# Optimization experiments

Measured on AMD Instinct MI355X. Metric: run time of the kernel, lower is better.

## Reference

```python
import jax, jax.numpy as jnp
import numpy as np

N = 6144      # total residues (12 complexes x 512)
SEG = 512
NC = 14       # atom channels per residue
E = 64        # embed_size
HD = 128      # hidden_size
C = 25        # num_classes
K = 9         # k_neighbors
L = 3         # n_layers
ROUNDS = 3    # iter_round


def _forward(X, S, batch_id, embed, W_in, b_in, channel_w, eW1, eb1, eW2, eb2, cW1, cb1, cW2, cb2, nW1, nb1, nW2, nb2, mW1, mb1, mW2, mb2, oW1, ob1, oW2, ob2):
    n = X.shape[0]
    silu = jax.nn.silu
    # pairs in different complexes (or self) are never neighbors
    cross = (batch_id[:, None] != batch_id[None, :]) | jnp.eye(n, dtype=bool)
    Hmem = None
    H = None
    for t in range(ROUNDS):
        H0 = embed[S]                                    # residue embedding [N,E]
        if Hmem is not None:                             # keep_memory: memory_ffn(H_prev)
            m = silu(Hmem) @ mW1 + mb1
            H0 = H0 + (silu(m) @ mW2 + mb2)
        H = H0 @ W_in + b_in                             # [N,HD]
        # dynamic KNN edge construction on current CA coordinates (_knn_edges)
        ca = X[:, 1]                                     # [N,3]
        d2 = jnp.sum((ca[:, None, :] - ca[None, :, :]) ** 2, -1)
        d2 = jnp.where(cross, 1e9, d2)
        _, nbr = jax.lax.top_k(-d2, K)                   # [N,K] neighbor indices
        for l in range(L):                               # AMEGNN / AMEncoder layers
            Hj = H[nbr]                                  # gather [N,K,HD]
            Xj = X[nbr]                                  # gather [N,K,NC,3]
            diff = X[:, None] - Xj                       # [N,K,NC,3]
            # channel-weighted radial feature
            radial = jnp.einsum('nkcd,nkcd,c->nk', diff, diff, channel_w)[..., None]
            Hi = jnp.broadcast_to(H[:, None], Hj.shape)
            ein = jnp.concatenate([Hi, Hj, radial], -1)  # [N,K,2HD+1]
            msg = silu(silu(ein @ eW1[l] + eb1[l]) @ eW2[l] + eb2[l])
            scale = silu(msg @ cW1[l] + cb1[l]) @ cW2[l] + cb2[l]     # [N,K,1]
            X = X + jnp.mean(diff * scale[..., None], axis=1)        # equivariant coord update
            agg = jnp.sum(msg, axis=1)                   # scatter-sum over neighbors [N,HD]
            H = H + silu(jnp.concatenate([H, agg], -1) @ nW1[l] + nb1[l]) @ nW2[l] + nb2[l]
        Hmem = H
    logits = silu(silu(H) @ oW1 + ob1) @ oW2 + ob2       # ffn_residue
    return logits, X


def setup_inputs() -> dict:
    key = jax.random.key(0)
    ks = jax.random.split(key, 16)
    r = lambda i, shape, s=0.05: jax.random.normal(ks[i], shape, dtype=jnp.float32) * s
    return {
        'X': jax.random.normal(ks[0], (N, NC, 3), dtype=jnp.float32) * 3.0,
        'S': jax.random.randint(ks[1], (N,), 0, C),
        'batch_id': jnp.arange(N, dtype=jnp.int32) // SEG,
        'embed': r(2, (C, E), 1.0),
        'W_in': r(3, (E, HD)), 'b_in': jnp.zeros((HD,), jnp.float32),
        'channel_w': jax.random.uniform(ks[4], (NC,), dtype=jnp.float32),
        'eW1': r(5, (L, 2 * HD + 1, HD)), 'eb1': jnp.zeros((L, HD), jnp.float32),
        'eW2': r(6, (L, HD, HD)), 'eb2': jnp.zeros((L, HD), jnp.float32),
        'cW1': r(7, (L, HD, HD)), 'cb1': jnp.zeros((L, HD), jnp.float32),
        'cW2': r(8, (L, HD, 1)), 'cb2': jnp.zeros((L, 1), jnp.float32),
        'nW1': r(9, (L, 2 * HD, HD)), 'nb1': jnp.zeros((L, HD), jnp.float32),
        'nW2': r(10, (L, HD, HD)), 'nb2': jnp.zeros((L, HD), jnp.float32),
        'mW1': r(11, (HD, HD)), 'mb1': jnp.zeros((HD,), jnp.float32),
        'mW2': r(12, (HD, E)), 'mb2': jnp.zeros((E,), jnp.float32),
        'oW1': r(13, (HD, HD)), 'ob1': jnp.zeros((HD,), jnp.float32),
        'oW2': r(14, (HD, C)), 'ob2': jnp.zeros((C,), jnp.float32),
    }


def reference(X, S, batch_id, embed, W_in, b_in, channel_w, eW1, eb1, eW2, eb2, cW1, cb1, cW2, cb2, nW1, nb1, nW2, nb2, mW1, mb1, mW2, mb2, oW1, ob1, oW2, ob2):
    return _forward(X, S, batch_id, embed, W_in, b_in, channel_w, eW1, eb1, eW2, eb2, cW1, cb1, cW2, cb2, nW1, nb1, nW2, nb2, mW1, mb1, mW2, mb2, oW1, ob1, oW2, ob2)
```

## Files before the change

kernel.cpp:

```cpp
#include <hip/hip_runtime.h>
#include <math.h>

#define NNODE 6144
#define SEG   512
#define NCH   14
#define XD    42
#define ED    64
#define HD    128
#define NCLS  25
#define KN    9
#define NPB   7
#define ROWS  64
#define EDGE_BLOCKS ((NNODE + NPB - 1) / NPB)

typedef __attribute__((ext_vector_type(8))) short short8;
typedef __attribute__((ext_vector_type(4))) short short4v;
typedef __attribute__((ext_vector_type(4))) float f32x4;

__device__ __forceinline__ float silu_f(float x) {
  return x / (1.0f + __expf(-x));
}
__device__ __forceinline__ short f2bf(float x) {
  unsigned u = __builtin_bit_cast(unsigned, x);
  unsigned r = (u + 0x7fffu + ((u >> 16) & 1u)) >> 16;
  return (short)r;
}
__device__ __forceinline__ float bf2f(short s) {
  unsigned u = ((unsigned)(unsigned short)s) << 16;
  return __builtin_bit_cast(float, u);
}
__device__ __forceinline__ f32x4 mfma16(short8 a, short8 b, f32x4 c) {
  return __builtin_amdgcn_mfma_f32_16x16x32_bf16(a, b, c, 0, 0, 0);
}
__device__ __forceinline__ int swz128(int row, int col) {
  return row * 128 + (col ^ ((row & 7) << 3));
}
__device__ __forceinline__ int swz256(int row, int col) {
  return row * 256 + (col ^ ((row & 7) << 3));
}
__device__ __forceinline__ int swz64(int row, int col) {
  return row * 64 + (col ^ ((row & 7) << 3));
}

#define EXOFF 344064
#define WBF_SHORTS (EXOFF + 32768)

__global__ __launch_bounds__(256) void prep_weights(
    const float* __restrict__ eW1, const float* __restrict__ eW2,
    const float* __restrict__ cW1, const float* __restrict__ nW1,
    const float* __restrict__ nW2, const float* __restrict__ mW1,
    const float* __restrict__ mW2, const float* __restrict__ W_in,
    short* __restrict__ out)
{
  const int idx = blockIdx.x * 256 + threadIdx.x;
  if (blockIdx.y == 15) {
    if (idx < 16384) {
      const int n = idx >> 7, k = idx & 127;
      out[EXOFF + idx] = f2bf(mW1[k * HD + n]);
    } else if (idx < 24576) {
      const int local = idx - 16384;
      const int n = local >> 7, k = local & 127;
      out[EXOFF + 16384 + local] = f2bf(mW2[k * ED + n]);
    } else if (idx < 32768) {
      const int local = idx - 24576;
      const int n = local >> 6, k = local & 63;
      out[EXOFF + 24576 + local] = f2bf(W_in[k * HD + n]);
    }
    return;
  }
  const int mat = blockIdx.y % 5, l = blockIdx.y / 5;
  const int K = (mat == 0 || mat == 3) ? 256 : 128;
  if (idx >= K * 128) return;
  const int n = idx / K, k = idx - n * K;
  const float* src;
  switch (mat) {
    case 0: src = eW1 + (size_t)l * 257 * 128; break;
    case 1: src = eW2 + (size_t)l * 128 * 128; break;
    case 2: src = cW1 + (size_t)l * 128 * 128; break;
    case 3: src = nW1 + (size_t)l * 256 * 128; break;
    default: src = nW2 + (size_t)l * 128 * 128; break;
  }
  const int dofs[5] = {0, 32768, 49152, 65536, 98304};
  out[(size_t)l * 114688 + dofs[mat] + idx] = f2bf(src[k * 128 + n]);
}

__global__ void copy_kernel(const float* __restrict__ src, float* __restrict__ dst, int n) {
  int i = blockIdx.x * blockDim.x + threadIdx.x;
  if (i < n) dst[i] = src[i];
}

__global__ __launch_bounds__(512) void h_init_mfma(
    const float* __restrict__ embed, const int* __restrict__ S,
    const short* __restrict__ W_inT, const float* __restrict__ b_in,
    const float* __restrict__ Hmem,
    const short* __restrict__ mW1T, const float* __restrict__ mb1,
    const short* __restrict__ mW2T, const float* __restrict__ mb2,
    const short* __restrict__ W1T0,
    float* __restrict__ Hout, short* __restrict__ PQ0)
{
  __shared__ __align__(16) short A[16 * HD];
  __shared__ __align__(16) short Bu[16 * HD];
  __shared__ __align__(16) short h0B[16 * ED];
  __shared__ __align__(16) short HB[16 * HD];
  const int t = threadIdx.x;
  const int m0 = blockIdx.x * 16;
  const int wid = t >> 6, lane = t & 63, lr = lane & 15, lk = lane >> 4;

  if (Hmem) {
    {
      const int r = t >> 5, c4 = t & 31;
      const float4 v = ((const float4*)Hmem)[(size_t)(m0 + r) * 32 + c4];
      short4v s;
      s.x = f2bf(silu_f(v.x)); s.y = f2bf(silu_f(v.y));
      s.z = f2bf(silu_f(v.z)); s.w = f2bf(silu_f(v.w));
      *(short4v*)&A[swz128(r, c4 * 4)] = s;
    }
    __syncthreads();
    {
      f32x4 acc[2] = {};
#pragma unroll
      for (int ks = 0; ks < 4; ++ks) {
        const int k0 = ks * 32 + lk * 8;
        const short8 a = *(const short8*)&A[swz128(lr, k0)];
#pragma unroll
        for (int ni = 0; ni < 2; ++ni) {
          const int c = (wid * 2 + ni) * 16 + lr;
          acc[ni] = mfma16(a, *(const short8*)(mW1T + c * 128 + k0), acc[ni]);
        }
      }
#pragma unroll
      for (int ni = 0; ni < 2; ++ni) {
        const int col = (wid * 2 + ni) * 16 + lr;
        const float bias = mb1[col];
#pragma unroll
        for (int g = 0; g < 4; ++g)
          Bu[swz128(lk * 4 + g, col)] = f2bf(silu_f(acc[ni][g] + bias));
      }
    }
    __syncthreads();
    if (wid < 4) {
      f32x4 acc = {};
#pragma unroll
      for (int ks = 0; ks < 4; ++ks) {
        const int k0 = ks * 32 + lk * 8;
        const short8 a = *(const short8*)&Bu[swz128(lr, k0)];
        const int c = wid * 16 + lr;
        acc = mfma16(a, *(const short8*)(mW2T + c * 128 + k0), acc);
      }
      const int col = wid * 16 + lr;
      const float bias = mb2[col];
#pragma unroll
      for (int g = 0; g < 4; ++g) {
        const int row = lk * 4 + g;
        h0B[swz64(row, col)] = f2bf(embed[S[m0 + row] * ED + col] + acc[g] + bias);
      }
    }
  } else {
    for (int idx = t; idx < 16 * ED; idx += 512) {
      const int row = idx >> 6, col = idx & 63;
      h0B[swz64(row, col)] = f2bf(embed[S[m0 + row] * ED + col]);
    }
  }
  __syncthreads();
  {
    f32x4 acc = {};
#pragma unroll
    for (int ks = 0; ks < 2; ++ks) {
      const int k0 = ks * 32 + lk * 8;
      const short8 a = *(const short8*)&h0B[swz64(lr, k0)];
      const int c = wid * 16 + lr;
      acc = mfma16(a, *(const short8*)(W_inT + c * 64 + k0), acc);
    }
    const int col = wid * 16 + lr;
    const float bias = b_in[col];
#pragma unroll
    for (int g = 0; g < 4; ++g) {
      const int row = lk * 4 + g;
      const float hv = acc[g] + bias;
      Hout[(size_t)(m0 + row) * HD + col] = hv;
      HB[swz128(row, col)] = f2bf(hv);
    }
  }
  __syncthreads();
  {
    f32x4 acc[2] = {};
#pragma unroll
    for (int ks = 0; ks < 4; ++ks) {
      const int k0 = ks * 32 + lk * 8;
      const short8 a = *(const short8*)&HB[swz128(lr, k0)];
#pragma unroll
      for (int ni = 0; ni < 2; ++ni) {
        const int c = (wid * 2 + ni) * 16 + lr;
        const short* bp = (c < HD) ? (W1T0 + c * 256 + k0)
                                   : (W1T0 + (c - HD) * 256 + HD + k0);
        acc[ni] = mfma16(a, *(const short8*)bp, acc[ni]);
      }
    }
#pragma unroll
    for (int ni = 0; ni < 2; ++ni) {
      const int c = (wid * 2 + ni) * 16 + lr;
#pragma unroll
      for (int g = 0; g < 4; ++g)
        PQ0[(size_t)(m0 + lk * 4 + g) * 256 + c] = f2bf(acc[ni][g]);
    }
  }
}

__global__ __launch_bounds__(512) void knn_kernel(const float* __restrict__ X,
                                                  int* __restrict__ nbr)
{
  const int w = threadIdx.x >> 6, lane = threadIdx.x & 63;
  const int i = blockIdx.x * 8 + w;
  const int base = (i / SEG) * SEG;

  const float cx = X[i * XD + 3], cy = X[i * XD + 4], cz = X[i * XD + 5];
  float dv[8];
  int   di[8];
#pragma unroll
  for (int q = 0; q < 8; ++q) {
    const int j = base + lane + q * 64;
    float dx = __fsub_rn(cx, X[j * XD + 3]);
    float dy = __fsub_rn(cy, X[j * XD + 4]);
    float dz = __fsub_rn(cz, X[j * XD + 5]);
    float d2 = __fadd_rn(__fadd_rn(__fmul_rn(dx, dx), __fmul_rn(dy, dy)), __fmul_rn(dz, dz));
    if (j == i) d2 = 1e9f;
    dv[q] = d2; di[q] = j;
  }
  for (int it = 0; it < KN; ++it) {
    float bv = dv[0]; int bi = di[0];
#pragma unroll
    for (int q = 1; q < 8; ++q)
      if (dv[q] < bv || (dv[q] == bv && di[q] < bi)) { bv = dv[q]; bi = di[q]; }
#pragma unroll
    for (int m = 1; m < 64; m <<= 1) {
      float ov = __shfl_xor(bv, m, 64);
      int   oi = __shfl_xor(bi, m, 64);
      if (ov < bv || (ov == bv && oi < bi)) { bv = ov; bi = oi; }
    }
    if (lane == 0) nbr[i * KN + it] = bi;
    const int rel = bi - base;
    const int oq = rel >> 6;
#pragma unroll
    for (int q = 0; q < 8; ++q)
      if (q == oq && (rel & 63) == lane) dv[q] = 3e38f;
  }
}

__global__ __launch_bounds__(512) void edge_layer_kernel(
    const float* __restrict__ Hin,  float* __restrict__ Hout,
    const float* __restrict__ Xin,  float* __restrict__ Xout,
    const int*   __restrict__ nbr,  const float* __restrict__ channel_w,
    const short* __restrict__ PQ,
    const float* __restrict__ eW1,  const float* __restrict__ eb1,
    const float* __restrict__ eb2,  const float* __restrict__ cb1,
    const float* __restrict__ cW2,  const float* __restrict__ cb2,
    const float* __restrict__ nb1,  const float* __restrict__ nb2,
    const short* __restrict__ W2T,  const short* __restrict__ C1T,
    const short* __restrict__ N1T,  const short* __restrict__ N2T,
    const short* __restrict__ W1Tn, short* __restrict__ PQn)
{
  __shared__ __align__(16) short bufA[ROWS * HD];
  __shared__ __align__(16) short bufB[ROWS * HD];
  __shared__ __align__(16) short nodeA[NPB * 256];
  __shared__ __align__(16) short uT[NPB * HD];
  __shared__ float diffS[ROWS][XD];
  __shared__ float scalePart[ROWS][4];
  __shared__ int   nbrS[ROWS];
  short* houtB = bufA;

  const int t  = threadIdx.x;
  const int n0 = blockIdx.x * NPB;
  const int nvalid = (NNODE - n0 < NPB) ? (NNODE - n0) : NPB;
  const int evalid = nvalid * KN;

  {
    const int row  = t >> 3;
    const int part = t & 7;
    const bool rvalid = row < evalid;
    const int nd = row / KN;
    const int jn = rvalid ? nbr[n0 * KN + row] : n0;
    if (part == 0) nbrS[row] = jn;

    float r = 0.f;
    {
      const float* xi = Xin + (size_t)(n0 + ((nd < nvalid) ? nd : 0)) * XD;
      const float* xj = Xin + (size_t)jn * XD;
#pragma unroll
      for (int ii = 0; ii < 6; ++ii) {
        const int e = part + ii * 8;
        if (e < XD) {
          float d = 0.f;
          if (rvalid) d = xi[e] - xj[e];
          diffS[row][e] = d;
          r = fmaf(channel_w[e / 3] * d, d, r);
        }
      }
    }
    r += __shfl_xor(r, 1, 64);
    r += __shfl_xor(r, 2, 64);
    r += __shfl_xor(r, 4, 64);

    if (t < NPB * (HD / 4)) {
      const int r2 = t >> 5, c4 = t & 31;
      float4 v = make_float4(0.f, 0.f, 0.f, 0.f);
      if (r2 < nvalid) v = ((const float4*)Hin)[(size_t)(n0 + r2) * 32 + c4];
      short4v s;
      s.x = f2bf(v.x); s.y = f2bf(v.y); s.z = f2bf(v.z); s.w = f2bf(v.w);
      *(short4v*)&nodeA[swz256(r2, c4 * 4)] = s;
    }

    const int inode = n0 + ((nd < nvalid) ? nd : 0);
    const short4v* PQv = (const short4v*)PQ;
    const float4* w2564 = (const float4*)(eW1 + 256 * HD);
    const float4* eb14 = (const float4*)eb1;
#pragma unroll
    for (int ii = 0; ii < 4; ++ii) {
      const int c4 = part + ii * 8;
      const short4v ps = PQv[(size_t)inode * 64 + c4];
      const short4v qs = PQv[(size_t)jn * 64 + 32 + c4];
      const float4 w = w2564[c4];
      const float4 bb = eb14[c4];
      short4v s;
      s.x = f2bf(silu_f(bf2f(ps.x) + bf2f(qs.x) + r * w.x + bb.x));
      s.y = f2bf(silu_f(bf2f(ps.y) + bf2f(qs.y) + r * w.y + bb.y));
      s.z = f2bf(silu_f(bf2f(ps.z) + bf2f(qs.z) + r * w.z + bb.z));
      s.w = f2bf(silu_f(bf2f(ps.w) + bf2f(qs.w) + r * w.w + bb.w));
      *(short4v*)&bufA[swz128(row, c4 * 4)] = s;
    }
  }
  __syncthreads();

  const int wid  = t >> 6;
  const int lane = t & 63;
  const int m2 = wid >> 2;
  const int n2 = wid & 3;
  const int lr = lane & 15;
  const int lk = lane >> 4;
  const int rA0 = (m2 * 2) * 16 + lr;
  const int rA1 = rA0 + 16;

  {
    f32x4 acc[2][2] = {};
    const short* b0p = W2T + ((n2 * 2) * 16 + lr) * 128;
    const short* b1p = b0p + 16 * 128;
#pragma unroll
    for (int ks = 0; ks < 4; ++ks) {
      const int k0 = ks * 32 + lk * 8;
      const short8 a0 = *(const short8*)&bufA[swz128(rA0, k0)];
      const short8 a1 = *(const short8*)&bufA[swz128(rA1, k0)];
      const short8 b0 = *(const short8*)(b0p + k0);
      const short8 b1 = *(const short8*)(b1p + k0);
      acc[0][0] = mfma16(a0, b0, acc[0][0]);
      acc[0][1] = mfma16(a0, b1, acc[0][1]);
      acc[1][0] = mfma16(a1, b0, acc[1][0]);
      acc[1][1] = mfma16(a1, b1, acc[1][1]);
    }
#pragma unroll
    for (int ni = 0; ni < 2; ++ni) {
      const int col = (n2 * 2 + ni) * 16 + lr;
      const float bias = eb2[col];
#pragma unroll
      for (int mi = 0; mi < 2; ++mi) {
        const int rb = (m2 * 2 + mi) * 16 + lk * 4;
#pragma unroll
        for (int g = 0; g < 4; ++g)
          bufB[swz128(rb + g, col)] = f2bf(silu_f(acc[mi][ni][g] + bias));
      }
    }
  }
  __syncthreads();

  {
    f32x4 acc[2][2] = {};
    const short* b0p = C1T + ((n2 * 2) * 16 + lr) * 128;
    const short* b1p = b0p + 16 * 128;
#pragma unroll
    for (int ks = 0; ks < 4; ++ks) {
      const int k0 = ks * 32 + lk * 8;
      const short8 a0 = *(const short8*)&bufB[swz128(rA0, k0)];
      const short8 a1 = *(const short8*)&bufB[swz128(rA1, k0)];
      const short8 b0 = *(const short8*)(b0p + k0);
      const short8 b1 = *(const short8*)(b1p + k0);
      acc[0][0] = mfma16(a0, b0, acc[0][0]);
      acc[0][1] = mfma16(a0, b1, acc[0][1]);
      acc[1][0] = mfma16(a1, b0, acc[1][0]);
      acc[1][1] = mfma16(a1, b1, acc[1][1]);
    }
    float p[2][4];
#pragma unroll
    for (int mi = 0; mi < 2; ++mi)
#pragma unroll
      for (int g = 0; g < 4; ++g) p[mi][g] = 0.f;
#pragma unroll
    for (int ni = 0; ni < 2; ++ni) {
      const int col = (n2 * 2 + ni) * 16 + lr;
      const float bias = cb1[col];
      const float wv = cW2[col];
#pragma unroll
      for (int mi = 0; mi < 2; ++mi)
#pragma unroll
        for (int g = 0; g < 4; ++g)
          p[mi][g] = fmaf(silu_f(acc[mi][ni][g] + bias), wv, p[mi][g]);
    }
#pragma unroll
    for (int m = 1; m < 16; m <<= 1) {
#pragma unroll
      for (int mi = 0; mi < 2; ++mi)
#pragma unroll
        for (int g = 0; g < 4; ++g)
          p[mi][g] += __shfl_xor(p[mi][g], m, 64);
    }
    if (lr == 0) {
#pragma unroll
      for (int mi = 0; mi < 2; ++mi)
#pragma unroll
        for (int g = 0; g < 4; ++g)
          scalePart[(m2 * 2 + mi) * 16 + lk * 4 + g][n2] = p[mi][g];
    }
  }
  for (int idx = t; idx < NPB * HD; idx += 512) {
    const int r2 = idx >> 7, col = idx & 127;
    float v = 0.f;
    if (r2 < nvalid) {
#pragma unroll
      for (int k = 0; k < KN; ++k) v += bf2f(bufB[swz128(r2 * KN + k, col)]);
    }
    nodeA[swz256(r2, col + HD)] = f2bf(v);
  }
  __syncthreads();

  {
    f32x4 acc = {};
    const short* bp = N1T + (wid * 16 + lr) * 256;
#pragma unroll
    for (int ks = 0; ks < 8; ++ks) {
      const int k0 = ks * 32 + lk * 8;
      short8 a = {0, 0, 0, 0, 0, 0, 0, 0};
      if (lr < NPB) a = *(const short8*)&nodeA[swz256(lr, k0)];
      const short8 b = *(const short8*)(bp + k0);
      acc = mfma16(a, b, acc);
    }
    const int col = wid * 16 + lr;
    const float bias = nb1[col];
#pragma unroll
    for (int g = 0; g < 4; ++g) {
      const int orow = lk * 4 + g;
      if (orow < NPB) uT[swz128(orow, col)] = f2bf(silu_f(acc[g] + bias));
    }
  }
  if (t < NPB * XD) {
    const int nd = t / XD, e = t - nd * XD;
    if (nd < nvalid) {
      const float c2 = cb2[0];
      float a = 0.f;
#pragma unroll
      for (int k = 0; k < KN; ++k) {
        const int r = nd * KN + k;
        const float sc = ((scalePart[r][0] + scalePart[r][1])
                        + (scalePart[r][2] + scalePart[r][3])) + c2;
        a = fmaf(diffS[r][e], sc, a);
      }
      const float xi = Xin[(size_t)n0 * XD + t];
      Xout[(size_t)n0 * XD + t] = xi + a / 9.0f;
    }
  }
  __syncthreads();

  {
    f32x4 acc = {};
    const short* bp = N2T + (wid * 16 + lr) * 128;
#pragma unroll
    for (int ks = 0; ks < 4; ++ks) {
      const int k0 = ks * 32 + lk * 8;
      short8 a = {0, 0, 0, 0, 0, 0, 0, 0};
      if (lr < NPB) a = *(const short8*)&uT[swz128(lr, k0)];
      const short8 b = *(const short8*)(bp + k0);
      acc = mfma16(a, b, acc);
    }
    const int col = wid * 16 + lr;
    const float bias = nb2[col];
#pragma unroll
    for (int g = 0; g < 4; ++g) {
      const int row = lk * 4 + g;
      if (row < nvalid) {
        const float hv = Hin[(size_t)(n0 + row) * HD + col] + acc[g] + bias;
        Hout[(size_t)(n0 + row) * HD + col] = hv;
        if (W1Tn) houtB[swz128(row, col)] = f2bf(hv);
      }
    }
  }

  if (W1Tn) {
    __syncthreads();
    f32x4 acc[2] = {};
#pragma unroll
    for (int ks = 0; ks < 4; ++ks) {
      const int k0 = ks * 32 + lk * 8;
      short8 a = {0, 0, 0, 0, 0, 0, 0, 0};
      if (lr < NPB) a = *(const short8*)&houtB[swz128(lr, k0)];
#pragma unroll
      for (int ni = 0; ni < 2; ++ni) {
        const int c = (wid * 2 + ni) * 16 + lr;
        const short* bp = (c < HD) ? (W1Tn + c * 256 + k0)
                                   : (W1Tn + (c - HD) * 256 + HD + k0);
        acc[ni] = mfma16(a, *(const short8*)bp, acc[ni]);
      }
    }
#pragma unroll
    for (int ni = 0; ni < 2; ++ni) {
      const int c = (wid * 2 + ni) * 16 + lr;
#pragma unroll
      for (int g = 0; g < 4; ++g) {
        const int row = lk * 4 + g;
        if (row < nvalid) PQn[(size_t)(n0 + row) * 256 + c] = f2bf(acc[ni][g]);
      }
    }
  }
}

__global__ __launch_bounds__(128) void out_kernel(
    const float* __restrict__ H, const float* __restrict__ X,
    const float* __restrict__ oW1, const float* __restrict__ ob1,
    const float* __restrict__ oW2, const float* __restrict__ ob2,
    float* __restrict__ out)
{
  __shared__ float hs[HD];
  __shared__ float u[HD];
  const int i = blockIdx.x, j = threadIdx.x;

  hs[j] = silu_f(H[i * HD + j]);
  __syncthreads();
  float a0 = 0.f, a1 = 0.f, a2 = 0.f, a3 = 0.f;
  for (int k = 0; k < HD; k += 4) {
    a0 = fmaf(hs[k + 0], oW1[(k + 0) * HD + j], a0);
    a1 = fmaf(hs[k + 1], oW1[(k + 1) * HD + j], a1);
    a2 = fmaf(hs[k + 2], oW1[(k + 2) * HD + j], a2);
    a3 = fmaf(hs[k + 3], oW1[(k + 3) * HD + j], a3);
  }
  u[j] = silu_f(ob1[j] + ((a0 + a1) + (a2 + a3)));
  __syncthreads();
  if (j < NCLS) {
    float o0 = 0.f, o1 = 0.f, o2 = 0.f, o3 = 0.f;
    for (int k = 0; k < HD; k += 4) {
      o0 = fmaf(u[k + 0], oW2[(k + 0) * NCLS + j], o0);
      o1 = fmaf(u[k + 1], oW2[(k + 1) * NCLS + j], o1);
      o2 = fmaf(u[k + 2], oW2[(k + 2) * NCLS + j], o2);
      o3 = fmaf(u[k + 3], oW2[(k + 3) * NCLS + j], o3);
    }
    out[i * NCLS + j] = ob2[j] + ((o0 + o1) + (o2 + o3));
  }
  if (j < XD) out[NNODE * NCLS + i * XD + j] = X[i * XD + j];
}

extern "C" void kernel_launch(void* const* d_in, const int* in_sizes, int n_in,
                              void* d_out, int out_size, void* d_ws, size_t ws_size,
                              hipStream_t stream)
{
  const float* X0       = (const float*)d_in[0];
  const int*   S        = (const int*)  d_in[1];
  const float* embed    = (const float*)d_in[3];
  const float* W_in     = (const float*)d_in[4];
  const float* b_in     = (const float*)d_in[5];
  const float* channelw = (const float*)d_in[6];
  const float* eW1      = (const float*)d_in[7];
  const float* eb1      = (const float*)d_in[8];
  const float* eW2      = (const float*)d_in[9];
  const float* eb2      = (const float*)d_in[10];
  const float* cW1      = (const float*)d_in[11];
  const float* cb1      = (const float*)d_in[12];
  const float* cW2      = (const float*)d_in[13];
  const float* cb2      = (const float*)d_in[14];
  const float* nW1      = (const float*)d_in[15];
  const float* nb1      = (const float*)d_in[16];
  const float* nW2      = (const float*)d_in[17];
  const float* nb2      = (const float*)d_in[18];
  const float* mW1      = (const float*)d_in[19];
  const float* mb1      = (const float*)d_in[20];
  const float* mW2      = (const float*)d_in[21];
  const float* mb2      = (const float*)d_in[22];
  const float* oW1      = (const float*)d_in[23];
  const float* ob1      = (const float*)d_in[24];
  const float* oW2      = (const float*)d_in[25];
  const float* ob2      = (const float*)d_in[26];

  char* ws = (char*)d_ws;
  const size_t HBYTES = (size_t)NNODE * HD * sizeof(float);
  const size_t XBYTES = (size_t)NNODE * XD * sizeof(float);
  const size_t NBRB   = (size_t)NNODE * KN * sizeof(int);
  const size_t WBFB   = (size_t)WBF_SHORTS * sizeof(short);
  const size_t PQB    = (size_t)NNODE * 256 * sizeof(short);
  float* Hb[2] = { (float*)(ws), (float*)(ws + HBYTES) };
  float* Xb[2] = { (float*)(ws + 2 * HBYTES), (float*)(ws + 2 * HBYTES + XBYTES) };
  int*   nbr   = (int*)(ws + 2 * HBYTES + 2 * XBYTES);
  short* Wbf   = (short*)(ws + 2 * HBYTES + 2 * XBYTES + NBRB);
  short* PQb[2] = { (short*)(ws + 2 * HBYTES + 2 * XBYTES + NBRB + WBFB),
                    (short*)(ws + 2 * HBYTES + 2 * XBYTES + NBRB + WBFB + PQB) };

  prep_weights<<<dim3(128, 16), 256, 0, stream>>>(eW1, eW2, cW1, nW1, nW2,
                                                  mW1, mW2, W_in, Wbf);
  copy_kernel<<<(NNODE * XD + 255) / 256, 256, 0, stream>>>(X0, Xb[0], NNODE * XD);

  int hc = 0, xc = 0;
  for (int t = 0; t < 3; ++t) {
    const float* Hmem = (t == 0) ? nullptr : Hb[hc];
    h_init_mfma<<<NNODE / 16, 512, 0, stream>>>(
        embed, S, Wbf + EXOFF + 24576, b_in, Hmem,
        Wbf + EXOFF, mb1, Wbf + EXOFF + 16384, mb2,
        Wbf , Hb[hc ^ 1], PQb[0]);
    hc ^= 1;
    knn_kernel<<<NNODE / 8, 512, 0, stream>>>(Xb[xc], nbr);
    for (int l = 0; l < 3; ++l) {
      const short* Wl = Wbf + (size_t)l * 114688;
      const short* Wn = (l < 2) ? (Wbf + (size_t)(l + 1) * 114688) : nullptr;
      const short* pqr = (l == 1) ? PQb[1] : PQb[0];
      short* pqw = (l == 0) ? PQb[1] : ((l == 1) ? PQb[0] : nullptr);
      edge_layer_kernel<<<EDGE_BLOCKS, 512, 0, stream>>>(
          Hb[hc], Hb[hc ^ 1], Xb[xc], Xb[xc ^ 1], nbr, channelw, pqr,
          eW1 + (size_t)l * 257 * HD, eb1 + (size_t)l * HD,
          eb2 + (size_t)l * HD,  cb1 + (size_t)l * HD,
          cW2 + (size_t)l * HD,  cb2 + (size_t)l,
          nb1 + (size_t)l * HD,  nb2 + (size_t)l * HD,
          Wl + 32768, Wl + 49152, Wl + 65536, Wl + 98304,
          Wn, pqw);
      hc ^= 1; xc ^= 1;
    }
  }
  out_kernel<<<NNODE, HD, 0, stream>>>(Hb[hc], Xb[xc], oW1, ob1, oW2, ob2, (float*)d_out);
}
```

Baseline: 541.7 us.

## Double edge-layer block to 14 nodes with 1024 threads and drop diff staging

Each edge-layer block now handles 14 nodes (128 edge rows) with 1024 threads instead of 7 nodes and 512 threads. This halves the block count and amortizes weight-fragment loads over twice as many rows. The shared diffS buffer is removed, and the coordinate update recomputes diffs from global X through the staged neighbor indices. That update now runs on the upper 8 waves while the lower 8 waves do the node MLP MFMA. The neighbor-sum reduction is vectorized to process bf16 pairs, and the next-layer PQ projection assigns one 16-column tile per wave. In exchange the kernel does extra global reloads and uses more registers per thread under the 1024-thread launch bound.

```diff
diff --git a/kernel.cpp b/kernel.cpp
--- a/kernel.cpp
+++ b/kernel.cpp
@@ -9,8 +9,8 @@
 #define HD    128
 #define NCLS  25
 #define KN    9
-#define NPB   7
-#define ROWS  64
+#define NPB   14
+#define ROWS  128
 #define EDGE_BLOCKS ((NNODE + NPB - 1) / NPB)
 
 typedef __attribute__((ext_vector_type(8))) short short8;
@@ -246,7 +246,7 @@
   }
 }
 
-__global__ __launch_bounds__(512) void edge_layer_kernel(
+__global__ __launch_bounds__(1024) void edge_layer_kernel(
     const float* __restrict__ Hin,  float* __restrict__ Hout,
     const float* __restrict__ Xin,  float* __restrict__ Xout,
     const int*   __restrict__ nbr,  const float* __restrict__ channel_w,
@@ -263,7 +263,6 @@
   __shared__ __align__(16) short bufB[ROWS * HD];
   __shared__ __align__(16) short nodeA[NPB * 256];
   __shared__ __align__(16) short uT[NPB * HD];
-  __shared__ float diffS[ROWS][XD];
   __shared__ float scalePart[ROWS][4];
   __shared__ int   nbrS[ROWS];
   short* houtB = bufA;
@@ -291,7 +290,6 @@
         if (e < XD) {
           float d = 0.f;
           if (rvalid) d = xi[e] - xj[e];
-          diffS[row][e] = d;
           r = fmaf(channel_w[e / 3] * d, d, r);
         }
       }
@@ -336,7 +334,7 @@
   const int n2 = wid & 3;
   const int lr = lane & 15;
   const int lk = lane >> 4;
-  const int rA0 = (m2 * 2) * 16 + lr;
+  const int rA0 = m2 * 32 + lr;
   const int rA1 = rA0 + 16;
 
   {
@@ -418,18 +416,24 @@
           scalePart[(m2 * 2 + mi) * 16 + lk * 4 + g][n2] = p[mi][g];
     }
   }
-  for (int idx = t; idx < NPB * HD; idx += 512) {
-    const int r2 = idx >> 7, col = idx & 127;
-    float v = 0.f;
+  if (t < NPB * (HD / 2)) {
+    const int r2 = t >> 6, cp = (t & 63) * 2;
+    float v0 = 0.f, v1 = 0.f;
     if (r2 < nvalid) {
 #pragma unroll
-      for (int k = 0; k < KN; ++k) v += bf2f(bufB[swz128(r2 * KN + k, col)]);
-    }
-    nodeA[swz256(r2, col + HD)] = f2bf(v);
-  }
-  __syncthreads();
-
-  {
+      for (int k = 0; k < KN; ++k) {
+        const unsigned w = *(const unsigned*)&bufB[swz128(r2 * KN + k, cp)];
+        v0 += bf2f((short)(w & 0xffffu));
+        v1 += bf2f((short)(w >> 16));
+      }
+    }
+    const unsigned lo = (unsigned short)f2bf(v0);
+    const unsigned hi = (unsigned short)f2bf(v1);
+    *(unsigned*)&nodeA[swz256(r2, cp + HD)] = lo | (hi << 16);
+  }
+  __syncthreads();
+
+  if (wid < 8) {
     f32x4 acc = {};
     const short* bp = N1T + (wid * 16 + lr) * 256;
 #pragma unroll
@@ -447,26 +451,28 @@
       const int orow = lk * 4 + g;
       if (orow < NPB) uT[swz128(orow, col)] = f2bf(silu_f(acc[g] + bias));
     }
-  }
-  if (t < NPB * XD) {
-    const int nd = t / XD, e = t - nd * XD;
-    if (nd < nvalid) {
-      const float c2 = cb2[0];
-      float a = 0.f;
-#pragma unroll
-      for (int k = 0; k < KN; ++k) {
-        const int r = nd * KN + k;
-        const float sc = ((scalePart[r][0] + scalePart[r][1])
-                        + (scalePart[r][2] + scalePart[r][3])) + c2;
-        a = fmaf(diffS[r][e], sc, a);
-      }
-      const float xi = Xin[(size_t)n0 * XD + t];
-      Xout[(size_t)n0 * XD + t] = xi + a / 9.0f;
-    }
-  }
-  __syncthreads();
-
-  {
+  } else {
+    const float c2 = cb2[0];
+    const int t2 = t - 512;
+    for (int idx = t2; idx < NPB * XD; idx += 512) {
+      const int nd = idx / XD, e = idx - nd * XD;
+      if (nd < nvalid) {
+        const float xi = Xin[(size_t)n0 * XD + idx];
+        float a = 0.f;
+#pragma unroll
+        for (int k = 0; k < KN; ++k) {
+          const int r = nd * KN + k;
+          const float sc = ((scalePart[r][0] + scalePart[r][1])
+                          + (scalePart[r][2] + scalePart[r][3])) + c2;
+          a = fmaf(xi - Xin[(size_t)nbrS[r] * XD + e], sc, a);
+        }
+        Xout[(size_t)n0 * XD + idx] = xi + a / 9.0f;
+      }
+    }
+  }
+  __syncthreads();
+
+  if (wid < 8) {
     f32x4 acc = {};
     const short* bp = N2T + (wid * 16 + lr) * 128;
 #pragma unroll
@@ -492,28 +498,21 @@
 
   if (W1Tn) {
     __syncthreads();
-    f32x4 acc[2] = {};
+    f32x4 acc = {};
+    const int c = wid * 16 + lr;
+    const short* bp = (c < HD) ? (W1Tn + c * 256)
+                               : (W1Tn + (c - HD) * 256 + HD);
 #pragma unroll
     for (int ks = 0; ks < 4; ++ks) {
       const int k0 = ks * 32 + lk * 8;
       short8 a = {0, 0, 0, 0, 0, 0, 0, 0};
       if (lr < NPB) a = *(const short8*)&houtB[swz128(lr, k0)];
-#pragma unroll
-      for (int ni = 0; ni < 2; ++ni) {
-        const int c = (wid * 2 + ni) * 16 + lr;
-        const short* bp = (c < HD) ? (W1Tn + c * 256 + k0)
-                                   : (W1Tn + (c - HD) * 256 + HD + k0);
-        acc[ni] = mfma16(a, *(const short8*)bp, acc[ni]);
-      }
-    }
-#pragma unroll
-    for (int ni = 0; ni < 2; ++ni) {
-      const int c = (wid * 2 + ni) * 16 + lr;
-#pragma unroll
-      for (int g = 0; g < 4; ++g) {
-        const int row = lk * 4 + g;
-        if (row < nvalid) PQn[(size_t)(n0 + row) * 256 + c] = f2bf(acc[ni][g]);
-      }
+      acc = mfma16(a, *(const short8*)(bp + k0), acc);
+    }
+#pragma unroll
+    for (int g = 0; g < 4; ++g) {
+      const int row = lk * 4 + g;
+      if (row < nvalid) PQn[(size_t)(n0 + row) * 256 + c] = f2bf(acc[g]);
     }
   }
 }
@@ -614,7 +613,7 @@
       const short* Wn = (l < 2) ? (Wbf + (size_t)(l + 1) * 114688) : nullptr;
       const short* pqr = (l == 1) ? PQb[1] : PQb[0];
       short* pqw = (l == 0) ? PQb[1] : ((l == 1) ? PQb[0] : nullptr);
-      edge_layer_kernel<<<EDGE_BLOCKS, 512, 0, stream>>>(
+      edge_layer_kernel<<<EDGE_BLOCKS, 1024, 0, stream>>>(
           Hb[hc], Hb[hc ^ 1], Xb[xc], Xb[xc ^ 1], nbr, channelw, pqr,
           eW1 + (size_t)l * 257 * HD, eb1 + (size_t)l * HD,
           eb2 + (size_t)l * HD,  cb1 + (size_t)l * HD,
```

After: 558.2 us. 1.03x slower.
